# Optimization experiments

Measured on AMD Instinct MI355X. Metric: run time of the kernel, lower is better.

## Reference

```python
import jax, jax.numpy as jnp
import numpy as np

B, L, K, D, S = 8, 1024, 1024, 128, 16  # batch, nodes, eigvecs, d_model(=d_inner), d_state
ABAR_EPS = 1e-3
BN_EPS = 1e-5


def setup_inputs() -> dict:
    key = jax.random.key(0)
    ks = jax.random.split(key, 10)
    x = jax.random.normal(ks[0], (B, L, D), jnp.float32)
    attn_mask = jnp.ones((B, L), jnp.bool_)
    EigVecs = jax.random.normal(ks[1], (B, L, K), jnp.float32)
    EigVals = jax.random.uniform(ks[2], (B, K), jnp.float32)
    # BatchNorm1d (eval mode) params
    bn_gamma = jnp.ones((D,), jnp.float32)
    bn_beta = jnp.zeros((D,), jnp.float32)
    bn_mean = jnp.zeros((D,), jnp.float32)
    bn_var = jnp.ones((D,), jnp.float32)
    # in_proj Linear(D, 2*D)
    W_in = jax.random.normal(ks[3], (D, 2 * D), jnp.float32) / np.float32(np.sqrt(D))
    b_in = jnp.zeros((2 * D,), jnp.float32)
    # SSM params
    log_Delta = np.float32(np.log(1e-3)) + np.float32(np.log(0.1) - np.log(1e-3)) * jax.random.uniform(ks[4], (1, D), jnp.float32)
    Bp = 0.01 * jax.random.normal(ks[5], (1, D, S), jnp.float32)
    Cp = 0.01 * jax.random.normal(ks[6], (1, D, S), jnp.float32)
    log_A_real = jnp.log(0.5 * jnp.ones((D, S), jnp.float32))
    A_imag = jnp.pi * jnp.broadcast_to(jnp.arange(D, dtype=jnp.float32)[:, None], (D, S))
    # out_proj Linear(D, D)
    W_out = jax.random.normal(ks[7], (D, D), jnp.float32) / np.float32(np.sqrt(D))
    b_out = jnp.zeros((D,), jnp.float32)
    return {
        "x": x, "attn_mask": attn_mask, "EigVecs": EigVecs, "EigVals": EigVals,
        "bn_gamma": bn_gamma, "bn_beta": bn_beta, "bn_mean": bn_mean, "bn_var": bn_var,
        "W_in": W_in, "b_in": b_in, "log_Delta": log_Delta, "Bp": Bp, "Cp": Cp,
        "log_A_real": log_A_real, "A_imag": A_imag, "W_out": W_out, "b_out": b_out,
    }


def reference(x, attn_mask, EigVecs, EigVals, bn_gamma, bn_beta, bn_mean, bn_var,
              W_in, b_in, log_Delta, Bp, Cp, log_A_real, A_imag, W_out, b_out):
    # --- eig preprocessing ---
    ev = 1.0 - EigVals[:, :, None, None]            # (B,K,1,1)
    ev = jnp.nan_to_num(ev)
    Q = jnp.nan_to_num(EigVecs)                      # (B,L,K)
    Q = Q / jnp.linalg.norm(Q, axis=-1, keepdims=True)
    Q = jnp.nan_to_num(Q)
    # --- in_proj: BatchNorm1d (eval) + Linear ---
    xb = (x - bn_mean) * (bn_gamma / jnp.sqrt(bn_var + BN_EPS)) + bn_beta
    h = xb @ W_in + b_in                             # (B,L,2D)
    x1, z = jnp.split(h, 2, axis=-1)                 # split [d_model, d_model]
    u = x1 * jax.nn.silu(z)                          # (B,L,D)
    # --- discretized SSM params ---
    delta = jnp.exp(log_Delta)                       # (1,D)
    A = -jnp.exp(log_A_real) + 1j * A_imag           # (D,S) complex
    Abar = jnp.exp(-ABAR_EPS + delta[..., None] * A) # (1,D,S) complex
    Bbar = delta[..., None] * Bp                     # (1,D,S)
    # --- graph Fourier transform ---
    QTX = jnp.einsum('blk,bld->bkd', Q, u)           # (B,K,D)
    QTXB = QTX[..., None] * Bbar                     # (B,K,D,S)
    lamA = ev * Abar[:, None]                        # (B,K,D,S) complex
    lamQ = jnp.real(lamA / (1.0 - lamA) * QTXB)      # A_complex & not BC_complex -> .real
    # --- inverse transform + C reduction (fused) ---
    yssm = jnp.einsum('blk,bkds,ds->bld', Q, lamQ, Cp[0])  # (B,L,D)
    y = jax.nn.silu(yssm) @ W_out + b_out
    return y
```

## Files before the change

### kernel.cpp

```cpp
#include <hip/hip_runtime.h>
#include <math.h>

#define B_ 8
#define L_ 1024
#define K_ 1024
#define D_ 128
#define S_ 16
#define DS_ (D_ * S_)
#define KS_ 4
#define CSL_ 256
#define NIT_ 8

typedef short bf16x8 __attribute__((ext_vector_type(8)));
typedef float f32x4 __attribute__((ext_vector_type(4)));
typedef __attribute__((address_space(1))) const unsigned int gu32;
typedef __attribute__((address_space(3))) unsigned int lu32;

__device__ inline unsigned short f2bf(float f) {
    unsigned int u = __float_as_uint(f);
    u = (u + 0x7fffu + ((u >> 16) & 1u)) >> 16;
    return (unsigned short)u;
}
__device__ inline float bf2f(unsigned short h) {
    return __uint_as_float(((unsigned int)h) << 16);
}

__device__ inline size_t bswz(int b, int c, int n) {
    return ((((size_t)b * 32 + (c >> 5)) * 4 + ((c >> 3) & 3)) * 128 + n) * 8;
}

__global__ void k_params(const float* __restrict__ log_Delta,
                         const float* __restrict__ Bp,
                         const float* __restrict__ Cp,
                         const float* __restrict__ log_A_real,
                         const float* __restrict__ A_imag,
                         float* __restrict__ par) {
    int i = blockIdx.x * blockDim.x + threadIdx.x;
    if (i >= DS_) return;
    int d = i >> 4;
    int s = i & 15;
    double delta = exp((double)log_Delta[d]);
    double Are = -exp((double)log_A_real[i]);
    double Aim = (double)A_imag[i];
    double mag = exp(-1e-3 + delta * Are);
    double ang = delta * Aim;
    int o = s * D_ + d;
    par[o]            = (float)(mag * cos(ang));
    par[DS_ + o]      = (float)(mag * sin(ang));
    par[2 * DS_ + o]  = (float)(delta * (double)Bp[i] * (double)Cp[i]);
}

__global__ __launch_bounds__(256) void k_rownorm(const float* __restrict__ E,
                                                 float* __restrict__ rn) {
    int row = blockIdx.x;
    const float4* p = (const float4*)(E + (size_t)row * K_);
    int t = threadIdx.x;
    float4 v = p[t];
    float s = v.x * v.x + v.y * v.y + v.z * v.z + v.w * v.w;
    #pragma unroll
    for (int off = 32; off > 0; off >>= 1) s += __shfl_down(s, off, 64);
    __shared__ float red[4];
    if ((t & 63) == 0) red[t >> 6] = s;
    __syncthreads();
    if (t == 0) rn[row] = 1.0f / sqrtf(red[0] + red[1] + red[2] + red[3]);
}

__global__ __launch_bounds__(256) void k_inproj(
    const float* __restrict__ x, const float* __restrict__ g,
    const float* __restrict__ beta, const float* __restrict__ mean,
    const float* __restrict__ var, const float* __restrict__ W_in,
    const float* __restrict__ b_in, const float* __restrict__ rn,
    unsigned short* __restrict__ uswH, unsigned short* __restrict__ uswL) {
    __shared__ float xb[16][128];
    int row0 = blockIdx.x * 16;
    int t = threadIdx.x;
    #pragma unroll
    for (int p = 0; p < 8; ++p) {
        int idx = t + p * 256;
        int dd = idx & 127, r = idx >> 7;
        float sc = g[dd] / sqrtf(var[dd] + 1e-5f);
        xb[r][dd] = (x[(size_t)(row0 + r) * D_ + dd] - mean[dd]) * sc + beta[dd];
    }
    __syncthreads();
    int j = t & 127, half = t >> 7;
    float acc1[8], acc2[8];
    #pragma unroll
    for (int r = 0; r < 8; ++r) { acc1[r] = 0.f; acc2[r] = 0.f; }
    #pragma unroll 4
    for (int dd = 0; dd < 128; ++dd) {
        float w1 = W_in[dd * 256 + j];
        float w2 = W_in[dd * 256 + 128 + j];
        #pragma unroll
        for (int r = 0; r < 8; ++r) {
            float xv = xb[half * 8 + r][dd];
            acc1[r] = fmaf(xv, w1, acc1[r]);
            acc2[r] = fmaf(xv, w2, acc2[r]);
        }
    }
    float b1 = b_in[j], b2 = b_in[128 + j];
    bf16x8 hv, lv;
    #pragma unroll
    for (int r = 0; r < 8; ++r) {
        int row = row0 + half * 8 + r;
        float x1 = acc1[r] + b1;
        float z  = acc2[r] + b2;
        float sig = 1.0f / (1.0f + __expf(-z));
        float uv = rn[row] * x1 * z * sig;
        unsigned short h = f2bf(uv);
        hv[r] = (short)h;
        lv[r] = (short)f2bf(uv - bf2f(h));
    }
    int b = row0 >> 10;
    int l0 = (row0 & 1023) + half * 8;
    size_t off = bswz(b, l0, j);
    *(bf16x8*)&uswH[off] = hv;
    *(bf16x8*)&uswL[off] = lv;
}

template<bool ATRANS>
__global__ __launch_bounds__(256, 2) void k_gemm(
    const float* __restrict__ Asrc,
    const unsigned short* __restrict__ BsrcH,
    const unsigned short* __restrict__ BsrcL,
    float* __restrict__ P) {
    __shared__ unsigned short sAh[64 * 40];
    __shared__ unsigned short sAl[64 * 40];
    __shared__ unsigned short sBh[4224];
    __shared__ unsigned short sBl[4224];
    int bx = blockIdx.x;
    int ks = bx & (KS_ - 1);
    int mt16 = (bx >> 2) & 15;
    int b = bx >> 6;
    int m0 = mt16 * 64;
    int cbase = ks * CSL_;
    const float* Ab = Asrc + (size_t)b * 1024 * 1024;
    int t = threadIdx.x;
    int wave = t >> 6, lane = t & 63;
    int fr = lane & 15, q = lane >> 4;
    int wn = wave * 32;
    f32x4 acc[4][2];
    #pragma unroll
    for (int i = 0; i < 4; ++i)
        #pragma unroll
        for (int j = 0; j < 2; ++j) acc[i][j] = (f32x4){0.f, 0.f, 0.f, 0.f};

    for (int it = 0; it < NIT_; ++it) {
        int cb = cbase + it * 32;
        if (ATRANS) {
            int m = t & 63, cg = t >> 6;
            float v[8];
            #pragma unroll
            for (int i = 0; i < 8; ++i)
                v[i] = Ab[(size_t)(cb + cg * 8 + i) * 1024 + m0 + m];
            bf16x8 hv, lv;
            #pragma unroll
            for (int i = 0; i < 8; ++i) {
                unsigned short h = f2bf(v[i]);
                hv[i] = (short)h;
                lv[i] = (short)f2bf(v[i] - bf2f(h));
            }
            int p = (cg + (m >> 3)) & 3;
            *(bf16x8*)&sAh[m * 40 + p * 8] = hv;
            *(bf16x8*)&sAl[m * 40 + p * 8] = lv;
        } else {
            int m = t >> 2, cg = t & 3;
            float4 v0 = *(const float4*)&Ab[(size_t)(m0 + m) * 1024 + cb + cg * 8];
            float4 v1 = *(const float4*)&Ab[(size_t)(m0 + m) * 1024 + cb + cg * 8 + 4];
            float v[8] = {v0.x, v0.y, v0.z, v0.w, v1.x, v1.y, v1.z, v1.w};
            bf16x8 hv, lv;
            #pragma unroll
            for (int i = 0; i < 8; ++i) {
                unsigned short h = f2bf(v[i]);
                hv[i] = (short)h;
                lv[i] = (short)f2bf(v[i] - bf2f(h));
            }
            int p = (cg + (m >> 3)) & 3;
            *(bf16x8*)&sAh[m * 40 + p * 8] = hv;
            *(bf16x8*)&sAl[m * 40 + p * 8] = lv;
        }
        {
            int ct = (cbase >> 5) + it;
            size_t src0 = (((size_t)(b * 32 + ct)) * 4) * 1024;
            #pragma unroll
            for (int j = 0; j < 4; ++j) {
                int s = wave + j * 4;
                int qq = s & 3, nh = (s >> 2) & 1, hl = s >> 3;
                const unsigned short* src =
                    (hl ? BsrcL : BsrcH) + src0 + ((size_t)qq * 128 + nh * 64 + lane) * 8;
                unsigned short* dst =
                    (hl ? sBl : sBh) + qq * 1032 + nh * 512;
                __builtin_amdgcn_global_load_lds((gu32*)src, (lu32*)dst, 16, 0, 0);
            }
        }
        __syncthreads();
        bf16x8 ah[4], al[4], bh[2], bl[2];
        #pragma unroll
        for (int mt = 0; mt < 4; ++mt) {
            int r = mt * 16 + fr;
            int p = (q + (r >> 3)) & 3;
            int off = r * 40 + p * 8;
            ah[mt] = *(const bf16x8*)&sAh[off];
            al[mt] = *(const bf16x8*)&sAl[off];
        }
        #pragma unroll
        for (int nt = 0; nt < 2; ++nt) {
            int off = q * 1032 + (wn + nt * 16 + fr) * 8;
            bh[nt] = *(const bf16x8*)&sBh[off];
            bl[nt] = *(const bf16x8*)&sBl[off];
        }
        #pragma unroll
        for (int mt = 0; mt < 4; ++mt)
            #pragma unroll
            for (int nt = 0; nt < 2; ++nt) {
                acc[mt][nt] = __builtin_amdgcn_mfma_f32_16x16x32_bf16(
                    ah[mt], bh[nt], acc[mt][nt], 0, 0, 0);
                acc[mt][nt] = __builtin_amdgcn_mfma_f32_16x16x32_bf16(
                    ah[mt], bl[nt], acc[mt][nt], 0, 0, 0);
                acc[mt][nt] = __builtin_amdgcn_mfma_f32_16x16x32_bf16(
                    al[mt], bh[nt], acc[mt][nt], 0, 0, 0);
            }
        __syncthreads();
    }
    float* Pb = P + ((size_t)(ks * B_ + b) * 1024 + m0) * 128;
    #pragma unroll
    for (int mt = 0; mt < 4; ++mt)
        #pragma unroll
        for (int nt = 0; nt < 2; ++nt) {
            int col = wn + nt * 16 + fr;
            #pragma unroll
            for (int r = 0; r < 4; ++r)
                Pb[(size_t)(mt * 16 + q * 4 + r) * 128 + col] = acc[mt][nt][r];
        }
}

__global__ __launch_bounds__(256) void k_gepi(
    const float* __restrict__ P, const float* __restrict__ EigVals,
    const float* __restrict__ par,
    unsigned short* __restrict__ GswH, unsigned short* __restrict__ GswL) {
    __shared__ float parS[3 * DS_];
    __shared__ float Gs[16][132];
    int t = threadIdx.x;
    for (int i = t; i < 3 * DS_; i += 256) parS[i] = par[i];
    __syncthreads();
    int bx = blockIdx.x;
    int kt = bx & 63, b = bx >> 6;
    int k0 = kt * 16;
    #pragma unroll
    for (int sub = 0; sub < 2; ++sub) {
        int k = (t >> 5) + sub * 8;
        int d4 = (t & 31) * 4;
        int row = b * 1024 + k0 + k;
        float4 s = {0.f, 0.f, 0.f, 0.f};
        #pragma unroll
        for (int sl = 0; sl < KS_; ++sl) {
            float4 v = *(const float4*)&P[((size_t)sl * 8192 + row) * 128 + d4];
            s.x += v.x; s.y += v.y; s.z += v.z; s.w += v.w;
        }
        float ev = 1.0f - EigVals[row];
        float qv[4] = {s.x, s.y, s.z, s.w};
        float o[4];
        #pragma unroll
        for (int c = 0; c < 4; ++c) {
            int dd = d4 + c;
            float w = 0.f;
            #pragma unroll
            for (int ss = 0; ss < S_; ++ss) {
                float arp = parS[ss * D_ + dd];
                float aip = parS[DS_ + ss * D_ + dd];
                float cc  = parS[2 * DS_ + ss * D_ + dd];
                float a = ev * arp, bi = ev * aip;
                float oma = 1.0f - a;
                float b2 = bi * bi;
                float num = fmaf(a, oma, -b2);
                float den = fmaf(oma, oma, b2);
                float r = __builtin_amdgcn_rcpf(den);
                r = r * (2.0f - den * r);
                w = fmaf(cc, num * r, w);
            }
            o[c] = qv[c] * w;
        }
        *(float4*)&Gs[k][d4] = (float4){o[0], o[1], o[2], o[3]};
    }
    __syncthreads();
    int d = t >> 1, kc = (t & 1) * 8;
    bf16x8 hv, lv;
    #pragma unroll
    for (int i = 0; i < 8; ++i) {
        float v = Gs[kc + i][d];
        unsigned short h = f2bf(v);
        hv[i] = (short)h;
        lv[i] = (short)f2bf(v - bf2f(h));
    }
    size_t off = bswz(b, k0 + kc, d);
    *(bf16x8*)&GswH[off] = hv;
    *(bf16x8*)&GswL[off] = lv;
}

__global__ __launch_bounds__(256) void k_out(
    const float* __restrict__ P, const float* __restrict__ rn,
    const float* __restrict__ W_out, const float* __restrict__ b_out,
    float* __restrict__ y) {
    __shared__ float Ys[16][128];
    int row0 = blockIdx.x * 16;
    int t = threadIdx.x;
    #pragma unroll
    for (int r = 0; r < 2; ++r) {
        int idx = t + r * 256;
        int rr = idx >> 5, d4 = (idx & 31) * 4;
        int grow = row0 + rr;
        float4 s = {0.f, 0.f, 0.f, 0.f};
        #pragma unroll
        for (int sl = 0; sl < KS_; ++sl) {
            float4 v = *(const float4*)&P[((size_t)sl * 8192 + grow) * 128 + d4];
            s.x += v.x; s.y += v.y; s.z += v.z; s.w += v.w;
        }
        float rv = rn[grow];
        float o[4] = {s.x * rv, s.y * rv, s.z * rv, s.w * rv};
        #pragma unroll
        for (int c = 0; c < 4; ++c) {
            float sig = 1.0f / (1.0f + __expf(-o[c]));
            Ys[rr][d4 + c] = o[c] * sig;
        }
    }
    __syncthreads();
    int j = t & 127, h = t >> 7;
    float a2[8];
    #pragma unroll
    for (int r = 0; r < 8; ++r) a2[r] = 0.f;
    for (int dd = 0; dd < 128; dd += 4) {
        float w0 = W_out[(dd + 0) * 128 + j];
        float w1 = W_out[(dd + 1) * 128 + j];
        float w2 = W_out[(dd + 2) * 128 + j];
        float w3 = W_out[(dd + 3) * 128 + j];
        #pragma unroll
        for (int r = 0; r < 8; ++r) {
            float4 yv = *(float4*)&Ys[h * 8 + r][dd];
            a2[r] = fmaf(yv.x, w0, a2[r]);
            a2[r] = fmaf(yv.y, w1, a2[r]);
            a2[r] = fmaf(yv.z, w2, a2[r]);
            a2[r] = fmaf(yv.w, w3, a2[r]);
        }
    }
    float bo = b_out[j];
    #pragma unroll
    for (int r = 0; r < 8; ++r)
        y[(size_t)(row0 + h * 8 + r) * D_ + j] = a2[r] + bo;
}

extern "C" void kernel_launch(void* const* d_in, const int* in_sizes, int n_in,
                              void* d_out, int out_size, void* d_ws, size_t ws_size,
                              hipStream_t stream) {
    const float* x          = (const float*)d_in[0];
    const float* EigVecs    = (const float*)d_in[2];
    const float* EigVals    = (const float*)d_in[3];
    const float* bn_gamma   = (const float*)d_in[4];
    const float* bn_beta    = (const float*)d_in[5];
    const float* bn_mean    = (const float*)d_in[6];
    const float* bn_var     = (const float*)d_in[7];
    const float* W_in       = (const float*)d_in[8];
    const float* b_in       = (const float*)d_in[9];
    const float* log_Delta  = (const float*)d_in[10];
    const float* Bp         = (const float*)d_in[11];
    const float* Cp         = (const float*)d_in[12];
    const float* log_A_real = (const float*)d_in[13];
    const float* A_imag     = (const float*)d_in[14];
    const float* W_out      = (const float*)d_in[15];
    const float* b_out      = (const float*)d_in[16];

    float* y = (float*)d_out;
    char* w = (char*)d_ws;
    float* rn            = (float*)(w);
    float* par           = (float*)(w + 32768);
    unsigned short* uswH = (unsigned short*)(w + 65536);
    unsigned short* uswL = (unsigned short*)(w + 65536 + (1u << 21));
    unsigned short* GswH = (unsigned short*)(w + 65536 + 2 * (1u << 21));
    unsigned short* GswL = (unsigned short*)(w + 65536 + 3 * (1u << 21));
    float* P             = (float*)(w + 65536 + 4 * (1u << 21));

    k_params<<<dim3(8), dim3(256), 0, stream>>>(log_Delta, Bp, Cp, log_A_real, A_imag, par);
    k_rownorm<<<dim3(B_ * L_), dim3(256), 0, stream>>>(EigVecs, rn);
    k_inproj<<<dim3(B_ * L_ / 16), dim3(256), 0, stream>>>(
        x, bn_gamma, bn_beta, bn_mean, bn_var, W_in, b_in, rn, uswH, uswL);
    k_gemm<true><<<dim3(16 * KS_ * B_), dim3(256), 0, stream>>>(EigVecs, uswH, uswL, P);
    k_gepi<<<dim3(B_ * 64), dim3(256), 0, stream>>>(P, EigVals, par, GswH, GswL);
    k_gemm<false><<<dim3(16 * KS_ * B_), dim3(256), 0, stream>>>(EigVecs, GswH, GswL, P);
    k_out<<<dim3(B_ * L_ / 16), dim3(256), 0, stream>>>(P, rn, W_out, b_out, y);
}
```

Before: 179.4 us.

## Fuse row-norm into in-proj, double split-K, prefetch next A tile

The row-norm kernel is merged into the in-projection kernel: each block reduces its 16 EigVecs rows itself and keeps the inverse norms in shared memory, which removes one launch and one global round-trip. The GEMM split-K factor goes from 4 to 8, giving more, shorter blocks, and launch bounds rise to allow 4 blocks per CU. The next A-tile is loaded from global into registers while the current tile is being computed, which hides load latency. In exchange, the partial-sum buffer and the reduction in the later kernels grow, and the higher occupancy target puts pressure on registers.

```diff
diff --git a/kernel.cpp b/kernel.cpp
--- a/kernel.cpp
+++ b/kernel.cpp
@@ -7,9 +7,9 @@
 #define D_ 128
 #define S_ 16
 #define DS_ (D_ * S_)
-#define KS_ 4
-#define CSL_ 256
-#define NIT_ 8
+#define KS_ 8
+#define CSL_ 128
+#define NIT_ 4
 
 typedef short bf16x8 __attribute__((ext_vector_type(8)));
 typedef float f32x4 __attribute__((ext_vector_type(4)));
@@ -50,30 +50,33 @@
     par[2 * DS_ + o]  = (float)(delta * (double)Bp[i] * (double)Cp[i]);
 }
 
-__global__ __launch_bounds__(256) void k_rownorm(const float* __restrict__ E,
-                                                 float* __restrict__ rn) {
-    int row = blockIdx.x;
-    const float4* p = (const float4*)(E + (size_t)row * K_);
-    int t = threadIdx.x;
-    float4 v = p[t];
-    float s = v.x * v.x + v.y * v.y + v.z * v.z + v.w * v.w;
-    #pragma unroll
-    for (int off = 32; off > 0; off >>= 1) s += __shfl_down(s, off, 64);
-    __shared__ float red[4];
-    if ((t & 63) == 0) red[t >> 6] = s;
-    __syncthreads();
-    if (t == 0) rn[row] = 1.0f / sqrtf(red[0] + red[1] + red[2] + red[3]);
-}
-
-__global__ __launch_bounds__(256) void k_inproj(
-    const float* __restrict__ x, const float* __restrict__ g,
-    const float* __restrict__ beta, const float* __restrict__ mean,
-    const float* __restrict__ var, const float* __restrict__ W_in,
-    const float* __restrict__ b_in, const float* __restrict__ rn,
+__global__ __launch_bounds__(256) void k_pre(
+    const float* __restrict__ E, const float* __restrict__ x,
+    const float* __restrict__ g, const float* __restrict__ beta,
+    const float* __restrict__ mean, const float* __restrict__ var,
+    const float* __restrict__ W_in, const float* __restrict__ b_in,
+    float* __restrict__ rn_out,
     unsigned short* __restrict__ uswH, unsigned short* __restrict__ uswL) {
     __shared__ float xb[16][128];
+    __shared__ float rsum[16];
+    __shared__ float rnS[16];
     int row0 = blockIdx.x * 16;
     int t = threadIdx.x;
+    {
+        int r = t >> 4, tt = t & 15;
+        const float4* Ep = (const float4*)(E + (size_t)(row0 + r) * K_);
+        float s = 0.f;
+        #pragma unroll
+        for (int i = 0; i < 16; ++i) {
+            float4 v = Ep[tt + i * 16];
+            s += v.x * v.x + v.y * v.y + v.z * v.z + v.w * v.w;
+        }
+        s += __shfl_xor(s, 8, 64);
+        s += __shfl_xor(s, 4, 64);
+        s += __shfl_xor(s, 2, 64);
+        s += __shfl_xor(s, 1, 64);
+        if (tt == 0) rsum[r] = s;
+    }
     #pragma unroll
     for (int p = 0; p < 8; ++p) {
         int idx = t + p * 256;
@@ -82,6 +85,12 @@
         xb[r][dd] = (x[(size_t)(row0 + r) * D_ + dd] - mean[dd]) * sc + beta[dd];
     }
     __syncthreads();
+    if (t < 16) {
+        float rv = 1.0f / sqrtf(rsum[t]);
+        rnS[t] = rv;
+        rn_out[row0 + t] = rv;
+    }
+    __syncthreads();
     int j = t & 127, half = t >> 7;
     float acc1[8], acc2[8];
     #pragma unroll
@@ -101,11 +110,11 @@
     bf16x8 hv, lv;
     #pragma unroll
     for (int r = 0; r < 8; ++r) {
-        int row = row0 + half * 8 + r;
+        int rr = half * 8 + r;
         float x1 = acc1[r] + b1;
         float z  = acc2[r] + b2;
         float sig = 1.0f / (1.0f + __expf(-z));
-        float uv = rn[row] * x1 * z * sig;
+        float uv = rnS[rr] * x1 * z * sig;
         unsigned short h = f2bf(uv);
         hv[r] = (short)h;
         lv[r] = (short)f2bf(uv - bf2f(h));
@@ -118,7 +127,7 @@
 }
 
 template<bool ATRANS>
-__global__ __launch_bounds__(256, 2) void k_gemm(
+__global__ __launch_bounds__(256, 4) void k_gemm(
     const float* __restrict__ Asrc,
     const unsigned short* __restrict__ BsrcH,
     const unsigned short* __restrict__ BsrcL,
@@ -129,8 +138,8 @@
     __shared__ unsigned short sBl[4224];
     int bx = blockIdx.x;
     int ks = bx & (KS_ - 1);
-    int mt16 = (bx >> 2) & 15;
-    int b = bx >> 6;
+    int mt16 = (bx >> 3) & 15;
+    int b = bx >> 7;
     int m0 = mt16 * 64;
     int cbase = ks * CSL_;
     const float* Ab = Asrc + (size_t)b * 1024 * 1024;
@@ -138,20 +147,28 @@
     int wave = t >> 6, lane = t & 63;
     int fr = lane & 15, q = lane >> 4;
     int wn = wave * 32;
+    int m_, cg_;
+    if (ATRANS) { m_ = t & 63; cg_ = t >> 6; }
+    else        { m_ = t >> 2; cg_ = t & 3; }
     f32x4 acc[4][2];
     #pragma unroll
     for (int i = 0; i < 4; ++i)
         #pragma unroll
         for (int j = 0; j < 2; ++j) acc[i][j] = (f32x4){0.f, 0.f, 0.f, 0.f};
 
+    float v[8];
+    if (ATRANS) {
+        #pragma unroll
+        for (int i = 0; i < 8; ++i)
+            v[i] = Ab[(size_t)(cbase + cg_ * 8 + i) * 1024 + m0 + m_];
+    } else {
+        *(float4*)&v[0] = *(const float4*)&Ab[(size_t)(m0 + m_) * 1024 + cbase + cg_ * 8];
+        *(float4*)&v[4] = *(const float4*)&Ab[(size_t)(m0 + m_) * 1024 + cbase + cg_ * 8 + 4];
+    }
+
+    #pragma unroll
     for (int it = 0; it < NIT_; ++it) {
-        int cb = cbase + it * 32;
-        if (ATRANS) {
-            int m = t & 63, cg = t >> 6;
-            float v[8];
-            #pragma unroll
-            for (int i = 0; i < 8; ++i)
-                v[i] = Ab[(size_t)(cb + cg * 8 + i) * 1024 + m0 + m];
+        {
             bf16x8 hv, lv;
             #pragma unroll
             for (int i = 0; i < 8; ++i) {
@@ -159,27 +176,12 @@
                 hv[i] = (short)h;
                 lv[i] = (short)f2bf(v[i] - bf2f(h));
             }
-            int p = (cg + (m >> 3)) & 3;
-            *(bf16x8*)&sAh[m * 40 + p * 8] = hv;
-            *(bf16x8*)&sAl[m * 40 + p * 8] = lv;
-        } else {
-            int m = t >> 2, cg = t & 3;
-            float4 v0 = *(const float4*)&Ab[(size_t)(m0 + m) * 1024 + cb + cg * 8];
-            float4 v1 = *(const float4*)&Ab[(size_t)(m0 + m) * 1024 + cb + cg * 8 + 4];
-            float v[8] = {v0.x, v0.y, v0.z, v0.w, v1.x, v1.y, v1.z, v1.w};
-            bf16x8 hv, lv;
-            #pragma unroll
-            for (int i = 0; i < 8; ++i) {
-                unsigned short h = f2bf(v[i]);
-                hv[i] = (short)h;
-                lv[i] = (short)f2bf(v[i] - bf2f(h));
-            }
-            int p = (cg + (m >> 3)) & 3;
-            *(bf16x8*)&sAh[m * 40 + p * 8] = hv;
-            *(bf16x8*)&sAl[m * 40 + p * 8] = lv;
+            int p = (cg_ + (m_ >> 3)) & 3;
+            *(bf16x8*)&sAh[m_ * 40 + p * 8] = hv;
+            *(bf16x8*)&sAl[m_ * 40 + p * 8] = lv;
         }
         {
-            int ct = (cbase >> 5) + it;
+            int ct = ks * 4 + it;
             size_t src0 = (((size_t)(b * 32 + ct)) * 4) * 1024;
             #pragma unroll
             for (int j = 0; j < 4; ++j) {
@@ -193,6 +195,17 @@
             }
         }
         __syncthreads();
+        if (it + 1 < NIT_) {
+            int cb = cbase + (it + 1) * 32;
+            if (ATRANS) {
+                #pragma unroll
+                for (int i = 0; i < 8; ++i)
+                    v[i] = Ab[(size_t)(cb + cg_ * 8 + i) * 1024 + m0 + m_];
+            } else {
+                *(float4*)&v[0] = *(const float4*)&Ab[(size_t)(m0 + m_) * 1024 + cb + cg_ * 8];
+                *(float4*)&v[4] = *(const float4*)&Ab[(size_t)(m0 + m_) * 1024 + cb + cg_ * 8 + 4];
+            }
+        }
         bf16x8 ah[4], al[4], bh[2], bl[2];
         #pragma unroll
         for (int mt = 0; mt < 4; ++mt) {
@@ -378,11 +391,10 @@
     float* P             = (float*)(w + 65536 + 4 * (1u << 21));
 
     k_params<<<dim3(8), dim3(256), 0, stream>>>(log_Delta, Bp, Cp, log_A_real, A_imag, par);
-    k_rownorm<<<dim3(B_ * L_), dim3(256), 0, stream>>>(EigVecs, rn);
-    k_inproj<<<dim3(B_ * L_ / 16), dim3(256), 0, stream>>>(
-        x, bn_gamma, bn_beta, bn_mean, bn_var, W_in, b_in, rn, uswH, uswL);
-    k_gemm<true><<<dim3(16 * KS_ * B_), dim3(256), 0, stream>>>(EigVecs, uswH, uswL, P);
+    k_pre<<<dim3(B_ * L_ / 16), dim3(256), 0, stream>>>(
+        EigVecs, x, bn_gamma, bn_beta, bn_mean, bn_var, W_in, b_in, rn, uswH, uswL);
+    k_gemm<true><<<dim3(KS_ * 16 * B_), dim3(256), 0, stream>>>(EigVecs, uswH, uswL, P);
     k_gepi<<<dim3(B_ * 64), dim3(256), 0, stream>>>(P, EigVals, par, GswH, GswL);
-    k_gemm<false><<<dim3(16 * KS_ * B_), dim3(256), 0, stream>>>(EigVecs, GswH, GswL, P);
+    k_gemm<false><<<dim3(KS_ * 16 * B_), dim3(256), 0, stream>>>(EigVecs, GswH, GswL, P);
     k_out<<<dim3(B_ * L_ / 16), dim3(256), 0, stream>>>(P, rn, W_out, b_out, y);
 }
```

Measured after the change: 177.1 us. No clear change (-1.3%).
